# Optimization experiments

Measured on AMD Instinct MI355X. Metric: run time of the kernel, lower is better.

The kernel has to match this reference:

```python
import jax, jax.numpy as jnp
from jax import lax
import numpy as np

SCALE = 1.0   # self.scale
EPS = 1e-12
CHUNK = 512   # points processed per chunk to bound [P,T,3] temporaries


def _closest_sqdist(p, a, b, c):
    """Squared distance from points p:[P,3] to triangles (a,b,c):[T,3] -> [P,T].
    Ericson's closest-point-on-triangle, fully vectorized."""
    ab = b - a
    ac = c - a
    bc = c - b
    ap = p[:, None, :] - a[None, :, :]
    bp = p[:, None, :] - b[None, :, :]
    cp = p[:, None, :] - c[None, :, :]
    d1 = jnp.einsum('td,ptd->pt', ab, ap)
    d2 = jnp.einsum('td,ptd->pt', ac, ap)
    d3 = jnp.einsum('td,ptd->pt', ab, bp)
    d4 = jnp.einsum('td,ptd->pt', ac, bp)
    d5 = jnp.einsum('td,ptd->pt', ab, cp)
    d6 = jnp.einsum('td,ptd->pt', ac, cp)
    va = d3 * d6 - d5 * d4
    vb = d5 * d2 - d1 * d6
    vc = d1 * d4 - d3 * d2

    def sdiv(n, d):  # NaN/Inf-safe division (branch is masked out by where anyway)
        return n / jnp.where(jnp.abs(d) < EPS, 1.0, d)

    t_ab = sdiv(d1, d1 - d3)[..., None]
    t_ac = sdiv(d2, d2 - d6)[..., None]
    t_bc = sdiv(d4 - d3, (d4 - d3) + (d5 - d6))[..., None]
    denom = va + vb + vc
    v_in = sdiv(vb, denom)[..., None]
    w_in = sdiv(vc, denom)[..., None]

    # base case: interior of the face; then overwrite with edge / vertex regions
    cl = a[None] + v_in * ab[None] + w_in * ac[None]
    cl = jnp.where(((va <= 0) & (d4 - d3 >= 0) & (d5 - d6 >= 0))[..., None],
                   b[None] + t_bc * bc[None], cl)   # edge BC
    cl = jnp.where(((vb <= 0) & (d2 >= 0) & (d6 <= 0))[..., None],
                   a[None] + t_ac * ac[None], cl)   # edge AC
    cl = jnp.where(((vc <= 0) & (d1 >= 0) & (d3 <= 0))[..., None],
                   a[None] + t_ab * ab[None], cl)   # edge AB
    cl = jnp.where(((d6 >= 0) & (d5 <= d6))[..., None], c[None], cl)  # vertex C
    cl = jnp.where(((d3 >= 0) & (d4 <= d3))[..., None], b[None], cl)  # vertex B
    cl = jnp.where(((d1 <= 0) & (d2 <= 0))[..., None], a[None], cl)   # vertex A
    diff = p[:, None, :] - cl
    return jnp.sum(diff * diff, axis=-1)


def setup_inputs():
    key = jax.random.key(0)
    k1, k2, k3 = jax.random.split(key, 3)
    vertices = jax.random.normal(k1, (4, 3, 16, 16, 16), dtype=jnp.float32)
    pc = jax.random.uniform(k2, (4, 4096, 3), dtype=jnp.float32)
    faces = jax.random.randint(k3, (8192, 3), 0, 4096, dtype=jnp.int32)
    return {"vertices": vertices, "pc": pc, "faces": faces}


def reference(vertices, pc, faces):
    B = vertices.shape[0]
    v = jax.nn.sigmoid(vertices)                     # self.normalization
    pos = jnp.moveaxis(v, 1, -1).reshape(B, -1, 3)   # permute(1,2,3,0).view(-1,3)
    pts = pc * SCALE                                 # _scale_points
    # pymesh path drops all-zero points; emulate with a mask (scaling keeps zeros zero)
    mask = jnp.any(pc != 0.0, axis=-1).astype(pts.dtype)  # [B,N]

    def per_batch(args):
        posb, pb, mb = args
        a = posb[faces[:, 0]]
        b = posb[faces[:, 1]]
        c = posb[faces[:, 2]]
        n_chunks = pb.shape[0] // CHUNK

        def chunk_min(pch):  # [CHUNK,3] -> [CHUNK] nearest sq-dist over all tris
            return jnp.min(_closest_sqdist(pch, a, b, c), axis=-1)

        d = lax.map(chunk_min, pb.reshape(n_chunks, CHUNK, 3)).reshape(-1)
        cnt = jnp.maximum(jnp.sum(mb), 1.0)
        return jnp.sum(d * mb) / cnt                 # mean(squared_distances)

    losses = lax.map(per_batch, (pos, pts, mask))    # [B]
    return jnp.mean(losses)
```

## Files before the change

kernel.cpp:

```cpp
#include <hip/hip_runtime.h>
#include <math.h>
#include <float.h>

#define NB 4
#define NP 4096
#define NT 8192
#define NS 64
#define TCH (NT/NS)
#define PBLK 4
#define GRID (NB*NS*PBLK)
#define TREC 20
#define EPSD 1e-12

typedef float f2 __attribute__((ext_vector_type(2)));

__device__ __forceinline__ float sigm(float x) { return 1.0f / (1.0f + expf(-x)); }
__device__ __forceinline__ float clamp01f(float x) {
  return __builtin_amdgcn_fmed3f(x, 0.0f, 1.0f);
}

__global__ __launch_bounds__(256) void prep_kernel(
    const float* __restrict__ verts, const int* __restrict__ faces,
    float* __restrict__ tri, float* __restrict__ out)
{
  int idx = blockIdx.x * 256 + threadIdx.x;
  if (idx == 0) out[0] = 0.0f;
  if (idx >= NB * NT) return;
  int b = idx >> 13;
  int t = idx & (NT - 1);
  int f0 = faces[3 * t + 0], f1 = faces[3 * t + 1], f2i = faces[3 * t + 2];
  const float* vv = verts + (size_t)b * 3 * NP;
  float ax = sigm(vv[f0]),  ay = sigm(vv[NP + f0]),  az = sigm(vv[2 * NP + f0]);
  float bx = sigm(vv[f1]),  by = sigm(vv[NP + f1]),  bz = sigm(vv[2 * NP + f1]);
  float cx = sigm(vv[f2i]), cy = sigm(vv[NP + f2i]), cz = sigm(vv[2 * NP + f2i]);
  float abx = bx - ax, aby = by - ay, abz = bz - az;
  float acx = cx - ax, acy = cy - ay, acz = cz - az;
  double aa = (double)abx * abx + (double)aby * aby + (double)abz * abz;
  double am = (double)abx * acx + (double)aby * acy + (double)abz * acz;
  double cc = (double)acx * acx + (double)acy * acy + (double)acz * acz;
  double den = aa * cc - am * am;
  double bb  = aa - 2.0 * am + cc;
  float raa  = (fabs(aa)  < EPSD) ? 1.0f : (float)(1.0 / aa);
  float rcc  = (fabs(cc)  < EPSD) ? 1.0f : (float)(1.0 / cc);
  float rbb  = (fabs(bb)  < EPSD) ? 1.0f : (float)(1.0 / bb);
  float rden = (fabs(den) < EPSD) ? 0.0f : (float)(1.0 / den);
  float* r = tri + (size_t)idx * TREC;
  r[0]  = ax;  r[1]  = ay;  r[2]  = az;
  r[3]  = abx; r[4]  = aby; r[5]  = abz;
  r[6]  = acx; r[7]  = acy; r[8]  = acz;
  r[9]  = (float)aa; r[10] = (float)am; r[11] = (float)cc;
  r[12] = raa; r[13] = rcc; r[14] = rbb; r[15] = rden;
  r[16] = (float)den; r[17] = (float)bb; r[18] = (float)(aa - am); r[19] = 0.0f;
}

__device__ __forceinline__ void tri_point(
    float4 r0, float4 r1, float4 r2, float4 r3, float4 r4,
    f2 px, f2 py, f2 pz, f2& mind)
{
  float abx = r0.w, aby = r1.x, abz = r1.y;
  float acx = r1.z, acy = r1.w, acz = r2.x;
  float aa = r2.y, am = r2.z, cc = r2.w;
  float raa = r3.x, rcc = r3.y, rbb = r3.z, rden = r3.w;
  float den = r4.x, bb = r4.y, k1 = r4.z;

  f2 apx = px - r0.x, apy = py - r0.y, apz = pz - r0.z;
  f2 d1   = apx * abx + apy * aby + apz * abz;
  f2 d2   = apx * acx + apy * acy + apz * acz;
  f2 apap = apx * apx + apy * apy + apz * apz;

  f2 vb = d1 * cc - d2 * am;
  f2 vc = d2 * aa - d1 * am;
  f2 va = den - vb - vc;
  f2 di = apap - (vb * d1 + vc * d2) * rden;

  f2 t2 = d1 + d1;
  f2 tab; tab.x = clamp01f(d1.x * raa); tab.y = clamp01f(d1.y * raa);
  f2 dAB = apap + tab * (tab * aa - t2);

  f2 t4 = d2 + d2;
  f2 tac; tac.x = clamp01f(d2.x * rcc); tac.y = clamp01f(d2.y * rcc);
  f2 dAC = apap + tac * (tac * cc - t4);

  f2 e = d2 - d1 + k1;
  f2 tbc; tbc.x = clamp01f(e.x * rbb); tbc.y = clamp01f(e.y * rbb);
  f2 distB = apap - t2 + aa;
  f2 e2 = e + e;
  f2 dBC = distB + tbc * (tbc * bb - e2);

  float m3x = fminf(fminf(dAB.x, dAC.x), dBC.x);
  float m3y = fminf(fminf(dAB.y, dAC.y), dBC.y);
  float sx  = fminf(fminf(vb.x, vc.x), va.x);
  float sy  = fminf(fminf(vb.y, vc.y), va.y);
  float dx = (sx > 0.0f) ? di.x : m3x;
  float dy = (sy > 0.0f) ? di.y : m3y;
  mind.x = fminf(mind.x, dx);
  mind.y = fminf(mind.y, dy);
}

__global__ __launch_bounds__(256) void dist_kernel(
    const float* __restrict__ tri, const float* __restrict__ pc,
    float* __restrict__ part)
{
  int bid  = blockIdx.x;
  int pblk = bid & (PBLK - 1);
  int s    = (bid >> 2) & (NS - 1);
  int b    = bid >> 8;
  int tid  = threadIdx.x;

  int p0 = pblk * 1024 + tid;
  const float* pp = pc + ((size_t)b * NP + p0) * 3;
  f2 pxA, pyA, pzA, pxB, pyB, pzB;
  pxA.x = pp[0];    pyA.x = pp[1];    pzA.x = pp[2];
  pxA.y = pp[768];  pyA.y = pp[769];  pzA.y = pp[770];
  pxB.x = pp[1536]; pyB.x = pp[1537]; pzB.x = pp[1538];
  pxB.y = pp[2304]; pyB.y = pp[2305]; pzB.y = pp[2306];
  f2 mindA, mindB;
  mindA.x = mindA.y = mindB.x = mindB.y = 3.0e38f;

  const float4* __restrict__ R =
      (const float4*)(tri + (size_t)(b * NT + s * TCH) * TREC);

  #pragma unroll 2
  for (int t = 0; t < TCH; ++t) {
    float4 r0 = R[0], r1 = R[1], r2 = R[2], r3 = R[3], r4 = R[4];
    R += 5;
    tri_point(r0, r1, r2, r3, r4, pxA, pyA, pzA, mindA);
    tri_point(r0, r1, r2, r3, r4, pxB, pyB, pzB, mindB);
  }

  float* dst = part + ((size_t)b * NS + s) * NP + p0;
  dst[0]   = fmaxf(mindA.x, 0.0f);
  dst[256] = fmaxf(mindA.y, 0.0f);
  dst[512] = fmaxf(mindB.x, 0.0f);
  dst[768] = fmaxf(mindB.y, 0.0f);
}

__global__ __launch_bounds__(1024) void reduce_kernel(
    const float* __restrict__ part, const float* __restrict__ pc,
    float* __restrict__ out)
{
  int b = blockIdx.x, tid = threadIdx.x;
  float sdm = 0.0f, sm = 0.0f;
  #pragma unroll
  for (int k = 0; k < 4; ++k) {
    int p = k * 1024 + tid;
    float m = 3.0e38f;
    #pragma unroll
    for (int s = 0; s < NS; ++s)
      m = fminf(m, part[((size_t)b * NS + s) * NP + p]);
    const float* q = pc + ((size_t)b * NP + p) * 3;
    bool nz = (q[0] != 0.0f) | (q[1] != 0.0f) | (q[2] != 0.0f);
    if (nz) { sdm += m; sm += 1.0f; }
  }
  for (int off = 32; off > 0; off >>= 1) {
    sdm += __shfl_down(sdm, off, 64);
    sm  += __shfl_down(sm,  off, 64);
  }
  __shared__ float s1[16], s2[16];
  int wv = tid >> 6, ln = tid & 63;
  if (ln == 0) { s1[wv] = sdm; s2[wv] = sm; }
  __syncthreads();
  if (wv == 0) {
    sdm = (ln < 16) ? s1[ln] : 0.0f;
    sm  = (ln < 16) ? s2[ln] : 0.0f;
    for (int off = 8; off > 0; off >>= 1) {
      sdm += __shfl_down(sdm, off, 64);
      sm  += __shfl_down(sm,  off, 64);
    }
    if (ln == 0) atomicAdd(out, 0.25f * (sdm / fmaxf(sm, 1.0f)));
  }
}

extern "C" void kernel_launch(void* const* d_in, const int* in_sizes, int n_in,
                              void* d_out, int out_size, void* d_ws, size_t ws_size,
                              hipStream_t stream) {
  const float* verts = (const float*)d_in[0];
  const float* pc    = (const float*)d_in[1];
  const int*   faces = (const int*)d_in[2];
  float* out = (float*)d_out;

  float* tri  = (float*)d_ws;
  float* part = tri + (size_t)NB * NT * TREC;

  prep_kernel<<<(NB * NT) / 256, 256, 0, stream>>>(verts, faces, tri, out);
  dist_kernel<<<GRID, 256, 0, stream>>>(tri, pc, part);
  reduce_kernel<<<NB, 1024, 0, stream>>>(part, pc, out);
}
```

Baseline: 182.2 us.

## Double triangle splits and parallelize final reduction across more blocks

```diff
diff --git a/kernel.cpp b/kernel.cpp
--- a/kernel.cpp
+++ b/kernel.cpp
@@ -5,10 +5,6 @@
 #define NB 4
 #define NP 4096
 #define NT 8192
-#define NS 64
-#define TCH (NT/NS)
-#define PBLK 4
-#define GRID (NB*NS*PBLK)
 #define TREC 20
 #define EPSD 1e-12
 
@@ -21,10 +17,12 @@
 
 __global__ __launch_bounds__(256) void prep_kernel(
     const float* __restrict__ verts, const int* __restrict__ faces,
-    float* __restrict__ tri, float* __restrict__ out)
+    float* __restrict__ tri, float* __restrict__ out,
+    unsigned int* __restrict__ cnt)
 {
   int idx = blockIdx.x * 256 + threadIdx.x;
   if (idx == 0) out[0] = 0.0f;
+  if (idx < NB) cnt[idx] = 0u;
   if (idx >= NB * NT) return;
   int b = idx >> 13;
   int t = idx & (NT - 1);
@@ -97,14 +95,16 @@
   mind.y = fminf(mind.y, dy);
 }
 
+template <int NSV, int SBITS>
 __global__ __launch_bounds__(256) void dist_kernel(
     const float* __restrict__ tri, const float* __restrict__ pc,
-    float* __restrict__ part)
-{
+    float* __restrict__ part, unsigned int* __restrict__ cnt)
+{
+  constexpr int TCH = NT / NSV;
   int bid  = blockIdx.x;
-  int pblk = bid & (PBLK - 1);
-  int s    = (bid >> 2) & (NS - 1);
-  int b    = bid >> 8;
+  int pblk = bid & 3;
+  int s    = (bid >> 2) & (NSV - 1);
+  int b    = bid >> (2 + SBITS);
   int tid  = threadIdx.x;
 
   int p0 = pblk * 1024 + tid;
@@ -128,46 +128,49 @@
     tri_point(r0, r1, r2, r3, r4, pxB, pyB, pzB, mindB);
   }
 
-  float* dst = part + ((size_t)b * NS + s) * NP + p0;
+  float* dst = part + ((size_t)b * NSV + s) * NP + p0;
   dst[0]   = fmaxf(mindA.x, 0.0f);
   dst[256] = fmaxf(mindA.y, 0.0f);
   dst[512] = fmaxf(mindB.x, 0.0f);
   dst[768] = fmaxf(mindB.y, 0.0f);
-}
-
-__global__ __launch_bounds__(1024) void reduce_kernel(
+
+  if (s == 0) {
+    int nz = 0;
+    nz += ((pxA.x != 0.0f) | (pyA.x != 0.0f) | (pzA.x != 0.0f)) ? 1 : 0;
+    nz += ((pxA.y != 0.0f) | (pyA.y != 0.0f) | (pzA.y != 0.0f)) ? 1 : 0;
+    nz += ((pxB.x != 0.0f) | (pyB.x != 0.0f) | (pzB.x != 0.0f)) ? 1 : 0;
+    nz += ((pxB.y != 0.0f) | (pyB.y != 0.0f) | (pzB.y != 0.0f)) ? 1 : 0;
+    for (int off = 32; off > 0; off >>= 1)
+      nz += __shfl_down(nz, off, 64);
+    if ((tid & 63) == 0) atomicAdd(&cnt[b], (unsigned int)nz);
+  }
+}
+
+template <int NSV>
+__global__ __launch_bounds__(256) void reduce_kernel(
     const float* __restrict__ part, const float* __restrict__ pc,
-    float* __restrict__ out)
-{
-  int b = blockIdx.x, tid = threadIdx.x;
-  float sdm = 0.0f, sm = 0.0f;
-  #pragma unroll
-  for (int k = 0; k < 4; ++k) {
-    int p = k * 1024 + tid;
-    float m = 3.0e38f;
-    #pragma unroll
-    for (int s = 0; s < NS; ++s)
-      m = fminf(m, part[((size_t)b * NS + s) * NP + p]);
-    const float* q = pc + ((size_t)b * NP + p) * 3;
-    bool nz = (q[0] != 0.0f) | (q[1] != 0.0f) | (q[2] != 0.0f);
-    if (nz) { sdm += m; sm += 1.0f; }
-  }
-  for (int off = 32; off > 0; off >>= 1) {
+    const unsigned int* __restrict__ cnt, float* __restrict__ out)
+{
+  int blk = blockIdx.x;
+  int b = blk >> 4;
+  int p = (blk & 15) * 256 + threadIdx.x;
+  float m = 3.0e38f;
+  #pragma unroll 16
+  for (int s = 0; s < NSV; ++s)
+    m = fminf(m, part[((size_t)b * NSV + s) * NP + p]);
+  const float* q = pc + ((size_t)b * NP + p) * 3;
+  bool nz = (q[0] != 0.0f) | (q[1] != 0.0f) | (q[2] != 0.0f);
+  float sdm = nz ? m : 0.0f;
+  for (int off = 32; off > 0; off >>= 1)
     sdm += __shfl_down(sdm, off, 64);
-    sm  += __shfl_down(sm,  off, 64);
-  }
-  __shared__ float s1[16], s2[16];
-  int wv = tid >> 6, ln = tid & 63;
-  if (ln == 0) { s1[wv] = sdm; s2[wv] = sm; }
+  __shared__ float s1[4];
+  int wv = threadIdx.x >> 6, ln = threadIdx.x & 63;
+  if (ln == 0) s1[wv] = sdm;
   __syncthreads();
-  if (wv == 0) {
-    sdm = (ln < 16) ? s1[ln] : 0.0f;
-    sm  = (ln < 16) ? s2[ln] : 0.0f;
-    for (int off = 8; off > 0; off >>= 1) {
-      sdm += __shfl_down(sdm, off, 64);
-      sm  += __shfl_down(sm,  off, 64);
-    }
-    if (ln == 0) atomicAdd(out, 0.25f * (sdm / fmaxf(sm, 1.0f)));
+  if (threadIdx.x == 0) {
+    float tot = s1[0] + s1[1] + s1[2] + s1[3];
+    float c = (float)cnt[b];
+    atomicAdd(out, 0.25f * tot / fmaxf(c, 1.0f));
   }
 }
 
@@ -179,10 +182,21 @@
   const int*   faces = (const int*)d_in[2];
   float* out = (float*)d_out;
 
-  float* tri  = (float*)d_ws;
-  float* part = tri + (size_t)NB * NT * TREC;
-
-  prep_kernel<<<(NB * NT) / 256, 256, 0, stream>>>(verts, faces, tri, out);
-  dist_kernel<<<GRID, 256, 0, stream>>>(tri, pc, part);
-  reduce_kernel<<<NB, 1024, 0, stream>>>(part, pc, out);
-}
+  float* tri = (float*)d_ws;
+  size_t tri_f = (size_t)NB * NT * TREC;
+
+  size_t need128 = (tri_f + (size_t)NB * 128 * NP + 64) * 4;
+  if (ws_size >= need128) {
+    float* part = tri + tri_f;
+    unsigned int* cnt = (unsigned int*)(part + (size_t)NB * 128 * NP);
+    prep_kernel<<<(NB * NT) / 256, 256, 0, stream>>>(verts, faces, tri, out, cnt);
+    dist_kernel<128, 7><<<NB * 128 * 4, 256, 0, stream>>>(tri, pc, part, cnt);
+    reduce_kernel<128><<<NB * 16, 256, 0, stream>>>(part, pc, cnt, out);
+  } else {
+    float* part = tri + tri_f;
+    unsigned int* cnt = (unsigned int*)(part + (size_t)NB * 64 * NP);
+    prep_kernel<<<(NB * NT) / 256, 256, 0, stream>>>(verts, faces, tri, out, cnt);
+    dist_kernel<64, 6><<<NB * 64 * 4, 256, 0, stream>>>(tri, pc, part, cnt);
+    reduce_kernel<64><<<NB * 16, 256, 0, stream>>>(part, pc, cnt, out);
+  }
+}
```

Measured after the change: 184.4 us. About the same (+1.2%).
